# Kernel optimization log

Measured on AMD Instinct MI355X. Metric: run time of the kernel, lower is better.

The kernel has to match this reference:

```python
import jax, jax.numpy as jnp
import numpy as np

N = 100000   # nodes
E = 1000000  # edges (before self-loops)
IN = 128     # in_channel
HID = 32     # hidden_channels
H1 = 8       # in_head
OUT = 40     # out_channel
NEG_SLOPE = 0.2


def setup_inputs() -> dict:
    key = jax.random.key(0)
    ks = jax.random.split(key, 12)
    s = 0.05
    return {
        "x0": jax.random.normal(ks[0], (N, IN), jnp.float32),
        "W1": jax.random.normal(ks[1], (IN, H1 * HID), jnp.float32) * s,
        "att_src1": jax.random.normal(ks[2], (H1, HID), jnp.float32) * s,
        "att_dst1": jax.random.normal(ks[3], (H1, HID), jnp.float32) * s,
        "b1": jnp.zeros((H1 * HID,), jnp.float32),
        "W2": jax.random.normal(ks[4], (H1 * HID, 1 * HID), jnp.float32) * s,
        "att_src2": jax.random.normal(ks[5], (1, HID), jnp.float32) * s,
        "att_dst2": jax.random.normal(ks[6], (1, HID), jnp.float32) * s,
        "b2": jnp.zeros((HID,), jnp.float32),
        "linW": jax.random.normal(ks[7], (HID, OUT), jnp.float32) * s,
        "linb": jnp.zeros((OUT,), jnp.float32),
        "edge_index": jax.random.randint(ks[8], (2, E), 0, N, dtype=jnp.int64),
    }


def gat_conv(x, src, dst, W, att_src, att_dst, bias, concat):
    # PyG GATConv (eval mode): per-head linear, edge attention, dst-softmax, scatter-add
    H, C = att_src.shape
    h = (x @ W).reshape(N, H, C)                       # [N,H,C]
    a_src = jnp.sum(h * att_src[None], axis=-1)        # [N,H]
    a_dst = jnp.sum(h * att_dst[None], axis=-1)        # [N,H]
    alpha = jax.nn.leaky_relu(a_src[src] + a_dst[dst], NEG_SLOPE)  # [Etot,H]
    m = jax.ops.segment_max(alpha, dst, num_segments=N)           # [N,H]
    ea = jnp.exp(alpha - m[dst])
    denom = jax.ops.segment_sum(ea, dst, num_segments=N)
    w = ea / jnp.clip(denom, 1e-16, None)[dst]          # [Etot,H]
    out = jax.ops.segment_sum(w[:, :, None] * h[src], dst, num_segments=N)  # [N,H,C]
    out = out.reshape(N, H * C) if concat else jnp.mean(out, axis=1)
    return out + bias


def reference(x0, W1, att_src1, att_dst1, b1, W2, att_src2, att_dst2, b2, linW, linb, edge_index):
    # add self-loops (PyG add_self_loops=True default)
    loop = jnp.arange(N, dtype=edge_index.dtype)
    src = jnp.concatenate([edge_index[0], loop])
    dst = jnp.concatenate([edge_index[1], loop])
    # dropout layers are no-ops in eval mode
    x1 = gat_conv(x0, src, dst, W1, att_src1, att_dst1, b1, concat=True)   # [N, 8*HID]
    x2 = jax.nn.relu(x1)
    x2 = gat_conv(x2, src, dst, W2, att_src2, att_dst2, b2, concat=False)  # [N, HID]
    return x2 @ linW + linb                                                 # [N, OUT]
```

## Files before the change

### kernel.cpp

```cpp
#include <hip/hip_runtime.h>

#define N 100000
#define E 1000000
#define ETOT 1100000
#define NB1 391
#define NBE 4297

typedef __attribute__((ext_vector_type(8))) short bf16x8;
typedef __attribute__((ext_vector_type(4))) float f32x4;

__device__ __forceinline__ float lrelu(float x) { return x > 0.f ? x : 0.2f * x; }
__device__ __forceinline__ unsigned short f2b(float x) {
    unsigned u = __float_as_uint(x);
    return (unsigned short)((u + 0x7FFFu + ((u >> 16) & 1u)) >> 16);
}
__device__ __forceinline__ float b2f(unsigned short v) {
    return __uint_as_float(((unsigned)v) << 16);
}

__global__ __launch_bounds__(256) void prep_kernel(const int* __restrict__ ei,
                                                   int* __restrict__ hist,
                                                   const float* __restrict__ W1,
                                                   const float* __restrict__ W2,
                                                   const float* __restrict__ att_src1,
                                                   const float* __restrict__ att_dst1,
                                                   unsigned short* __restrict__ W1T,
                                                   unsigned short* __restrict__ W2T) {
    const int b = blockIdx.x;
    const int t = threadIdx.x;
    if (b < NBE) {
        const int e = b * 256 + t;
        if (e < ETOT) {
            int d = (e < E) ? ei[E + e] : (e - E);
            atomicAdd(&hist[d], 1);
        }
        return;
    }
    const int bb = b - NBE;
    if (bb < 128) {
        W1T[(size_t)t * 128 + bb] = f2b(W1[(size_t)bb * 256 + t]);
    } else if (bb < 160) {
        int n = bb - 128;
        W2T[(size_t)n * 256 + t] = f2b(W2[(size_t)t * 32 + n]);
    } else {
        int idx = (bb - 160) * 256 + t;
        int col = idx >> 7;
        int k = idx & 127;
        int h = col & 7;
        const float* att = (col < 8) ? att_src1 : att_dst1;
        float acc = 0.f;
#pragma unroll 8
        for (int j = 0; j < 32; j++) acc += W1[(size_t)k * 256 + h * 32 + j] * att[h * 32 + j];
        W1T[(size_t)(256 + col) * 128 + k] = f2b(acc);
    }
}

__global__ __launch_bounds__(256) void scan1_kernel(const int* __restrict__ hist,
                                                    int* __restrict__ rofs,
                                                    int* __restrict__ bsum) {
    __shared__ int sm[256];
    const int t = threadIdx.x;
    const int i = blockIdx.x * 256 + t;
    int v = (i < N) ? hist[i] : 0;
    sm[t] = v;
    __syncthreads();
#pragma unroll
    for (int off = 1; off < 256; off <<= 1) {
        int x = (t >= off) ? sm[t - off] : 0;
        __syncthreads();
        sm[t] += x;
        __syncthreads();
    }
    if (i < N) rofs[i] = sm[t] - v;
    if (t == 255) bsum[blockIdx.x] = sm[255];
}

__global__ __launch_bounds__(512) void scan2_kernel(int* __restrict__ bsum) {
    __shared__ int sm[512];
    const int t = threadIdx.x;
    int v = (t < NB1) ? bsum[t] : 0;
    sm[t] = v;
    __syncthreads();
#pragma unroll
    for (int off = 1; off < 512; off <<= 1) {
        int x = (t >= off) ? sm[t - off] : 0;
        __syncthreads();
        sm[t] += x;
        __syncthreads();
    }
    if (t < NB1) bsum[t] = sm[t] - v;
}

__global__ __launch_bounds__(256) void scan3_kernel(int* __restrict__ rofs,
                                                    const int* __restrict__ bsum,
                                                    int* __restrict__ cursor) {
    const int i = blockIdx.x * 256 + threadIdx.x;
    if (i < N) {
        int r = rofs[i] + bsum[blockIdx.x];
        rofs[i] = r;
        cursor[i] = r;
    }
    if (i == 0) rofs[N] = ETOT;
}

__global__ __launch_bounds__(256) void scatter_kernel(const int* __restrict__ ei,
                                                      int* __restrict__ cursor,
                                                      int* __restrict__ esrc) {
    const int e = blockIdx.x * 256 + threadIdx.x;
    if (e >= ETOT) return;
    int s, d;
    if (e < E) { s = ei[e]; d = ei[E + e]; } else { s = d = e - E; }
    int pos = atomicAdd(&cursor[d], 1);
    esrc[pos] = s;
}

__global__ __launch_bounds__(256) void gemm1_kernel(const float* __restrict__ x0,
                                                    const unsigned short* __restrict__ W1T,
                                                    unsigned short* __restrict__ h1,
                                                    float* __restrict__ a_src,
                                                    float* __restrict__ a_dst) {
    const int wv = threadIdx.x >> 6;
    const int lane = threadIdx.x & 63;
    const int quad = lane >> 4, c = lane & 15;
    const int base_m = blockIdx.x * 128 + wv * 32;
    bf16x8 af[2][4];
#pragma unroll
    for (int mt = 0; mt < 2; mt++) {
        int row = base_m + mt * 16 + c;
        int rowc = row < N ? row : N - 1;
        const float* ap = x0 + (size_t)rowc * 128 + quad * 8;
#pragma unroll
        for (int ks = 0; ks < 4; ks++) {
            float4 lo = *(const float4*)(ap + ks * 32);
            float4 hi = *(const float4*)(ap + ks * 32 + 4);
            bf16x8 f;
            f[0] = (short)f2b(lo.x); f[1] = (short)f2b(lo.y);
            f[2] = (short)f2b(lo.z); f[3] = (short)f2b(lo.w);
            f[4] = (short)f2b(hi.x); f[5] = (short)f2b(hi.y);
            f[6] = (short)f2b(hi.z); f[7] = (short)f2b(hi.w);
            af[mt][ks] = f;
        }
    }
    for (int nt = 0; nt < 17; nt++) {
        f32x4 acc0 = {0.f, 0.f, 0.f, 0.f};
        f32x4 acc1 = {0.f, 0.f, 0.f, 0.f};
#pragma unroll
        for (int ks = 0; ks < 4; ks++) {
            bf16x8 bf = *(const bf16x8*)(W1T + (size_t)(nt * 16 + c) * 128 + ks * 32 + quad * 8);
            acc0 = __builtin_amdgcn_mfma_f32_16x16x32_bf16(af[0][ks], bf, acc0, 0, 0, 0);
            acc1 = __builtin_amdgcn_mfma_f32_16x16x32_bf16(af[1][ks], bf, acc1, 0, 0, 0);
        }
        if (nt < 16) {
            const int col = nt * 16 + c;
#pragma unroll
            for (int r = 0; r < 4; r++) {
                int row0 = base_m + quad * 4 + r;
                if (row0 < N) h1[(size_t)row0 * 256 + col] = f2b(acc0[r]);
                int row1 = base_m + 16 + quad * 4 + r;
                if (row1 < N) h1[(size_t)row1 * 256 + col] = f2b(acc1[r]);
            }
        } else {
            float* dst = (c < 8) ? a_src : a_dst;
            int hh = c & 7;
#pragma unroll
            for (int r = 0; r < 4; r++) {
                int row0 = base_m + quad * 4 + r;
                if (row0 < N) dst[(size_t)row0 * 8 + hh] = acc0[r];
                int row1 = base_m + 16 + quad * 4 + r;
                if (row1 < N) dst[(size_t)row1 * 8 + hh] = acc1[r];
            }
        }
    }
}

__global__ __launch_bounds__(256) void seg1_kernel(const int* __restrict__ esrc,
                                                   const int* __restrict__ rofs,
                                                   const float* __restrict__ a_src,
                                                   const float* __restrict__ a_dst,
                                                   const unsigned short* __restrict__ h1,
                                                   const float* __restrict__ b1,
                                                   unsigned short* __restrict__ x2) {
    const int n = (blockIdx.x * 256 + threadIdx.x) >> 6;
    const int lane = threadIdx.x & 63;
    const int h = lane >> 3;
    const int rs = rofs[n], re = rofs[n + 1];
    const float ad = a_dst[(size_t)n * 8 + h];
    float d0 = 0.f, d1 = 0.f, d2 = 0.f, d3 = 0.f;
    float4 A0 = {0, 0, 0, 0}, A1 = {0, 0, 0, 0}, A2 = {0, 0, 0, 0}, A3 = {0, 0, 0, 0};
    for (int j0 = rs; j0 < re; j0 += 4) {
        const int cl = re - 1;
        int s0 = esrc[j0];
        int s1 = esrc[j0 + 1 < re ? j0 + 1 : cl];
        int s2 = esrc[j0 + 2 < re ? j0 + 2 : cl];
        int s3 = esrc[j0 + 3 < re ? j0 + 3 : cl];
        float as0 = a_src[(size_t)s0 * 8 + h];
        float as1 = a_src[(size_t)s1 * 8 + h];
        float as2 = a_src[(size_t)s2 * 8 + h];
        float as3 = a_src[(size_t)s3 * 8 + h];
        ushort4 hb0 = ((const ushort4*)(h1 + (size_t)s0 * 256))[lane];
        ushort4 hb1 = ((const ushort4*)(h1 + (size_t)s1 * 256))[lane];
        ushort4 hb2 = ((const ushort4*)(h1 + (size_t)s2 * 256))[lane];
        ushort4 hb3 = ((const ushort4*)(h1 + (size_t)s3 * 256))[lane];
        float w0 = __expf(lrelu(as0 + ad));
        float w1 = (j0 + 1 < re) ? __expf(lrelu(as1 + ad)) : 0.f;
        float w2 = (j0 + 2 < re) ? __expf(lrelu(as2 + ad)) : 0.f;
        float w3 = (j0 + 3 < re) ? __expf(lrelu(as3 + ad)) : 0.f;
        d0 += w0; d1 += w1; d2 += w2; d3 += w3;
        A0.x += w0 * b2f(hb0.x); A0.y += w0 * b2f(hb0.y); A0.z += w0 * b2f(hb0.z); A0.w += w0 * b2f(hb0.w);
        A1.x += w1 * b2f(hb1.x); A1.y += w1 * b2f(hb1.y); A1.z += w1 * b2f(hb1.z); A1.w += w1 * b2f(hb1.w);
        A2.x += w2 * b2f(hb2.x); A2.y += w2 * b2f(hb2.y); A2.z += w2 * b2f(hb2.z); A2.w += w2 * b2f(hb2.w);
        A3.x += w3 * b2f(hb3.x); A3.y += w3 * b2f(hb3.y); A3.z += w3 * b2f(hb3.z); A3.w += w3 * b2f(hb3.w);
    }
    float den = (d0 + d1) + (d2 + d3);
    float4 acc;
    acc.x = (A0.x + A1.x) + (A2.x + A3.x);
    acc.y = (A0.y + A1.y) + (A2.y + A3.y);
    acc.z = (A0.z + A1.z) + (A2.z + A3.z);
    acc.w = (A0.w + A1.w) + (A2.w + A3.w);
    const float inv = 1.0f / den;
    float4 bb = ((const float4*)b1)[lane];
    float vx = acc.x * inv + bb.x, vy = acc.y * inv + bb.y;
    float vz = acc.z * inv + bb.z, vw = acc.w * inv + bb.w;
    vx = vx > 0.f ? vx : 0.f; vy = vy > 0.f ? vy : 0.f;
    vz = vz > 0.f ? vz : 0.f; vw = vw > 0.f ? vw : 0.f;
    ushort4 o = {f2b(vx), f2b(vy), f2b(vz), f2b(vw)};
    ((ushort4*)(x2 + (size_t)n * 256))[lane] = o;
}

__global__ __launch_bounds__(256) void gemm2_kernel(const unsigned short* __restrict__ x2,
                                                    const unsigned short* __restrict__ W2T,
                                                    const float* __restrict__ att_src2,
                                                    const float* __restrict__ att_dst2,
                                                    unsigned short* __restrict__ h2,
                                                    float* __restrict__ a_src2,
                                                    float* __restrict__ a_dst2) {
    const int wv = threadIdx.x >> 6;
    const int lane = threadIdx.x & 63;
    const int quad = lane >> 4, c = lane & 15;
    const int base_m = blockIdx.x * 128 + wv * 32;
    f32x4 acc[2][2] = {{{0, 0, 0, 0}, {0, 0, 0, 0}}, {{0, 0, 0, 0}, {0, 0, 0, 0}}};
#pragma unroll
    for (int ks = 0; ks < 8; ks++) {
        bf16x8 b0 = *(const bf16x8*)(W2T + (size_t)c * 256 + ks * 32 + quad * 8);
        bf16x8 b1 = *(const bf16x8*)(W2T + (size_t)(16 + c) * 256 + ks * 32 + quad * 8);
#pragma unroll
        for (int mt = 0; mt < 2; mt++) {
            int row = base_m + mt * 16 + c;
            int rowc = row < N ? row : N - 1;
            bf16x8 a = *(const bf16x8*)(x2 + (size_t)rowc * 256 + ks * 32 + quad * 8);
            acc[mt][0] = __builtin_amdgcn_mfma_f32_16x16x32_bf16(a, b0, acc[mt][0], 0, 0, 0);
            acc[mt][1] = __builtin_amdgcn_mfma_f32_16x16x32_bf16(a, b1, acc[mt][1], 0, 0, 0);
        }
    }
    float as0 = att_src2[c], as1 = att_src2[16 + c];
    float ad0 = att_dst2[c], ad1 = att_dst2[16 + c];
#pragma unroll
    for (int mt = 0; mt < 2; mt++) {
#pragma unroll
        for (int r = 0; r < 4; r++) {
            int row = base_m + mt * 16 + quad * 4 + r;
            float v0 = acc[mt][0][r], v1 = acc[mt][1][r];
            float ps = v0 * as0 + v1 * as1;
            float pd = v0 * ad0 + v1 * ad1;
#pragma unroll
            for (int off = 1; off < 16; off <<= 1) {
                ps += __shfl_xor(ps, off, 64);
                pd += __shfl_xor(pd, off, 64);
            }
            if (row < N) {
                h2[(size_t)row * 32 + c] = f2b(v0);
                h2[(size_t)row * 32 + 16 + c] = f2b(v1);
                if (c == 0) { a_src2[row] = ps; a_dst2[row] = pd; }
            }
        }
    }
}

__global__ __launch_bounds__(256) void seg2_kernel(const int* __restrict__ esrc,
                                                   const int* __restrict__ rofs,
                                                   const float* __restrict__ a_src2,
                                                   const float* __restrict__ a_dst2,
                                                   const unsigned short* __restrict__ h2,
                                                   const float* __restrict__ b2,
                                                   const float* __restrict__ linW,
                                                   const float* __restrict__ linb,
                                                   float* __restrict__ out) {
    __shared__ float lws[32 * 40];
    __shared__ float vbuf[8][32];
    const int t = threadIdx.x;
    for (int i = t; i < 1280; i += 256) lws[i] = linW[i];
    const int n8 = t >> 5;
    const int c = t & 31;
    const int n = blockIdx.x * 8 + n8;
    const int rs = rofs[n], re = rofs[n + 1];
    const float ad = a_dst2[n];
    float d[8] = {0, 0, 0, 0, 0, 0, 0, 0};
    float A[8] = {0, 0, 0, 0, 0, 0, 0, 0};
    for (int j0 = rs; j0 < re; j0 += 8) {
        int sidx[8];
#pragma unroll
        for (int k = 0; k < 8; k++) {
            int j = j0 + k;
            sidx[k] = esrc[j < re ? j : re - 1];
        }
        unsigned short hb[8];
        float as[8];
#pragma unroll
        for (int k = 0; k < 8; k++) {
            hb[k] = h2[(size_t)sidx[k] * 32 + c];
            as[k] = a_src2[sidx[k]];
        }
#pragma unroll
        for (int k = 0; k < 8; k++) {
            float w = (j0 + k < re) ? __expf(lrelu(as[k] + ad)) : 0.f;
            d[k] += w;
            A[k] += w * b2f(hb[k]);
        }
    }
    float den = ((d[0] + d[1]) + (d[2] + d[3])) + ((d[4] + d[5]) + (d[6] + d[7]));
    float acc = ((A[0] + A[1]) + (A[2] + A[3])) + ((A[4] + A[5]) + (A[6] + A[7]));
    vbuf[n8][c] = acc / den + b2[c];
    __syncthreads();
    for (int idx = t; idx < 320; idx += 256) {
        int nn = idx / 40, o = idx - nn * 40;
        float s = linb[o];
#pragma unroll
        for (int ci = 0; ci < 32; ci++) s += vbuf[nn][ci] * lws[ci * 40 + o];
        out[(size_t)blockIdx.x * 320 + idx] = s;
    }
}

extern "C" void kernel_launch(void* const* d_in, const int* in_sizes, int n_in,
                              void* d_out, int out_size, void* d_ws, size_t ws_size,
                              hipStream_t stream) {
    const float* x0       = (const float*)d_in[0];
    const float* W1       = (const float*)d_in[1];
    const float* att_src1 = (const float*)d_in[2];
    const float* att_dst1 = (const float*)d_in[3];
    const float* b1       = (const float*)d_in[4];
    const float* W2       = (const float*)d_in[5];
    const float* att_src2 = (const float*)d_in[6];
    const float* att_dst2 = (const float*)d_in[7];
    const float* b2       = (const float*)d_in[8];
    const float* linW     = (const float*)d_in[9];
    const float* linb     = (const float*)d_in[10];
    const int*   ei       = (const int*)d_in[11];
    float* out = (float*)d_out;
    float* ws  = (float*)d_ws;

    unsigned short* h1   = (unsigned short*)ws;
    unsigned short* x2   = (unsigned short*)(ws + 12800000);
    float* a_src1        = ws + 25600000;
    float* a_dst1        = ws + 26400000;
    unsigned short* h2   = (unsigned short*)(ws + 27200000);
    float* a_src2        = ws + 28800000;
    float* a_dst2        = ws + 28900000;
    unsigned short* W1T  = (unsigned short*)(ws + 29000000);
    unsigned short* W2T  = (unsigned short*)(ws + 29020000);
    int*   hist          = (int*)(ws + 29030000);
    int*   rofs          = (int*)(ws + 29130000);
    int*   cursor        = (int*)(ws + 29240000);
    int*   bsum          = (int*)(ws + 29340000);
    int*   esrc          = (int*)(ws + 29341000);

    hipMemsetAsync(hist, 0, (size_t)N * 4, stream);

    prep_kernel<<<NBE + 168, 256, 0, stream>>>(ei, hist, W1, W2, att_src1, att_dst1, W1T, W2T);
    scan1_kernel<<<NB1, 256, 0, stream>>>(hist, rofs, bsum);
    scan2_kernel<<<1, 512, 0, stream>>>(bsum);
    scan3_kernel<<<NB1, 256, 0, stream>>>(rofs, bsum, cursor);
    scatter_kernel<<<(ETOT + 255) / 256, 256, 0, stream>>>(ei, cursor, esrc);

    gemm1_kernel<<<(N + 127) / 128, 256, 0, stream>>>(x0, W1T, h1, a_src1, a_dst1);
    seg1_kernel<<<N / 4, 256, 0, stream>>>(esrc, rofs, a_src1, a_dst1, h1, b1, x2);
    gemm2_kernel<<<(N + 127) / 128, 256, 0, stream>>>(x2, W2T, att_src2, att_dst2, h2, a_src2, a_dst2);
    seg2_kernel<<<N / 8, 256, 0, stream>>>(esrc, rofs, a_src2, a_dst2, h2, b2, linW, linb, out);
}
```

Measured before the change: 437.4 us.

## Cooperatively load edge indices and attention weights across lanes in segment kernels

```diff
diff --git a/kernel.cpp b/kernel.cpp
--- a/kernel.cpp
+++ b/kernel.cpp
@@ -182,41 +182,42 @@
                                                    unsigned short* __restrict__ x2) {
     const int n = (blockIdx.x * 256 + threadIdx.x) >> 6;
     const int lane = threadIdx.x & 63;
-    const int h = lane >> 3;
-    const int rs = rofs[n], re = rofs[n + 1];
-    const float ad = a_dst[(size_t)n * 8 + h];
-    float d0 = 0.f, d1 = 0.f, d2 = 0.f, d3 = 0.f;
-    float4 A0 = {0, 0, 0, 0}, A1 = {0, 0, 0, 0}, A2 = {0, 0, 0, 0}, A3 = {0, 0, 0, 0};
-    for (int j0 = rs; j0 < re; j0 += 4) {
-        const int cl = re - 1;
-        int s0 = esrc[j0];
-        int s1 = esrc[j0 + 1 < re ? j0 + 1 : cl];
-        int s2 = esrc[j0 + 2 < re ? j0 + 2 : cl];
-        int s3 = esrc[j0 + 3 < re ? j0 + 3 : cl];
-        float as0 = a_src[(size_t)s0 * 8 + h];
-        float as1 = a_src[(size_t)s1 * 8 + h];
-        float as2 = a_src[(size_t)s2 * 8 + h];
-        float as3 = a_src[(size_t)s3 * 8 + h];
-        ushort4 hb0 = ((const ushort4*)(h1 + (size_t)s0 * 256))[lane];
-        ushort4 hb1 = ((const ushort4*)(h1 + (size_t)s1 * 256))[lane];
-        ushort4 hb2 = ((const ushort4*)(h1 + (size_t)s2 * 256))[lane];
-        ushort4 hb3 = ((const ushort4*)(h1 + (size_t)s3 * 256))[lane];
-        float w0 = __expf(lrelu(as0 + ad));
-        float w1 = (j0 + 1 < re) ? __expf(lrelu(as1 + ad)) : 0.f;
-        float w2 = (j0 + 2 < re) ? __expf(lrelu(as2 + ad)) : 0.f;
-        float w3 = (j0 + 3 < re) ? __expf(lrelu(as3 + ad)) : 0.f;
-        d0 += w0; d1 += w1; d2 += w2; d3 += w3;
-        A0.x += w0 * b2f(hb0.x); A0.y += w0 * b2f(hb0.y); A0.z += w0 * b2f(hb0.z); A0.w += w0 * b2f(hb0.w);
-        A1.x += w1 * b2f(hb1.x); A1.y += w1 * b2f(hb1.y); A1.z += w1 * b2f(hb1.z); A1.w += w1 * b2f(hb1.w);
-        A2.x += w2 * b2f(hb2.x); A2.y += w2 * b2f(hb2.y); A2.z += w2 * b2f(hb2.z); A2.w += w2 * b2f(hb2.w);
-        A3.x += w3 * b2f(hb3.x); A3.y += w3 * b2f(hb3.y); A3.z += w3 * b2f(hb3.z); A3.w += w3 * b2f(hb3.w);
-    }
-    float den = (d0 + d1) + (d2 + d3);
-    float4 acc;
-    acc.x = (A0.x + A1.x) + (A2.x + A3.x);
-    acc.y = (A0.y + A1.y) + (A2.y + A3.y);
-    acc.z = (A0.z + A1.z) + (A2.z + A3.z);
-    acc.w = (A0.w + A1.w) + (A2.w + A3.w);
+    const int e_pa = lane >> 3;
+    const int h_pa = lane & 7;
+    const int hB = lane >> 3;
+    const int rs = __builtin_amdgcn_readfirstlane(rofs[n]);
+    const int re = __builtin_amdgcn_readfirstlane(rofs[n + 1]);
+    const float ad_pa = a_dst[(size_t)n * 8 + h_pa];
+    float dsum = 0.f;
+    float4 Aa = {0, 0, 0, 0}, Ab = {0, 0, 0, 0};
+    for (int j0 = rs; j0 < re; j0 += 8) {
+        int jm = j0 + e_pa;
+        int jc = jm < re ? jm : re - 1;
+        int s8 = esrc[jc];
+        float av = a_src[(size_t)s8 * 8 + h_pa];
+        float ex = __expf(lrelu(av + ad_pa));
+        float w = (jm < re) ? ex : 0.f;
+        dsum += w;
+#pragma unroll
+        for (int e = 0; e < 8; e++) {
+            if ((e & 3) == 0 && j0 + e >= re) break;
+            float wb = __shfl(w, e * 8 + hB, 64);
+            int se = __builtin_amdgcn_readlane(s8, e * 8);
+            ushort4 hb = ((const ushort4*)(h1 + (size_t)se * 256))[lane];
+            if (e & 1) {
+                Ab.x += wb * b2f(hb.x); Ab.y += wb * b2f(hb.y);
+                Ab.z += wb * b2f(hb.z); Ab.w += wb * b2f(hb.w);
+            } else {
+                Aa.x += wb * b2f(hb.x); Aa.y += wb * b2f(hb.y);
+                Aa.z += wb * b2f(hb.z); Aa.w += wb * b2f(hb.w);
+            }
+        }
+    }
+    dsum += __shfl_xor(dsum, 8, 64);
+    dsum += __shfl_xor(dsum, 16, 64);
+    dsum += __shfl_xor(dsum, 32, 64);
+    float den = __shfl(dsum, hB, 64);
+    float4 acc = {Aa.x + Ab.x, Aa.y + Ab.y, Aa.z + Ab.z, Aa.w + Ab.w};
     const float inv = 1.0f / den;
     float4 bb = ((const float4*)b1)[lane];
     float vx = acc.x * inv + bb.x, vy = acc.y * inv + bb.y;
@@ -286,47 +287,50 @@
                                                    const float* __restrict__ linb,
                                                    float* __restrict__ out) {
     __shared__ float lws[32 * 40];
-    __shared__ float vbuf[8][32];
+    __shared__ float vbuf[4][32];
     const int t = threadIdx.x;
     for (int i = t; i < 1280; i += 256) lws[i] = linW[i];
-    const int n8 = t >> 5;
-    const int c = t & 31;
-    const int n = blockIdx.x * 8 + n8;
-    const int rs = rofs[n], re = rofs[n + 1];
+    const int wv = t >> 6;
+    const int lane = t & 63;
+    const int n = blockIdx.x * 4 + wv;
+    const int rs = __builtin_amdgcn_readfirstlane(rofs[n]);
+    const int re = __builtin_amdgcn_readfirstlane(rofs[n + 1]);
     const float ad = a_dst2[n];
-    float d[8] = {0, 0, 0, 0, 0, 0, 0, 0};
-    float A[8] = {0, 0, 0, 0, 0, 0, 0, 0};
-    for (int j0 = rs; j0 < re; j0 += 8) {
-        int sidx[8];
-#pragma unroll
-        for (int k = 0; k < 8; k++) {
-            int j = j0 + k;
-            sidx[k] = esrc[j < re ? j : re - 1];
-        }
-        unsigned short hb[8];
-        float as[8];
-#pragma unroll
-        for (int k = 0; k < 8; k++) {
-            hb[k] = h2[(size_t)sidx[k] * 32 + c];
-            as[k] = a_src2[sidx[k]];
-        }
-#pragma unroll
-        for (int k = 0; k < 8; k++) {
-            float w = (j0 + k < re) ? __expf(lrelu(as[k] + ad)) : 0.f;
-            d[k] += w;
-            A[k] += w * b2f(hb[k]);
-        }
-    }
-    float den = ((d[0] + d[1]) + (d[2] + d[3])) + ((d[4] + d[5]) + (d[6] + d[7]));
-    float acc = ((A[0] + A[1]) + (A[2] + A[3])) + ((A[4] + A[5]) + (A[6] + A[7]));
-    vbuf[n8][c] = acc / den + b2[c];
+    const int ec = lane >> 5;
+    const int c = lane & 31;
+    float dsum = 0.f;
+    float A = 0.f;
+    for (int j0 = rs; j0 < re; j0 += 64) {
+        int jm = j0 + lane;
+        int jc = jm < re ? jm : re - 1;
+        int s = esrc[jc];
+        float av = a_src2[s];
+        float ex = __expf(lrelu(av + ad));
+        float w = (jm < re) ? ex : 0.f;
+        dsum += w;
+        int cnt = re - j0; if (cnt > 64) cnt = 64;
+        for (int e = 0; e < cnt; e += 2) {
+            float wb = __shfl(w, e + ec, 64);
+            int sb = __shfl(s, e + ec, 64);
+            unsigned short hb = h2[(size_t)sb * 32 + c];
+            A += wb * b2f(hb);
+        }
+    }
+    A += __shfl_xor(A, 32, 64);
+    dsum += __shfl_xor(dsum, 1, 64);
+    dsum += __shfl_xor(dsum, 2, 64);
+    dsum += __shfl_xor(dsum, 4, 64);
+    dsum += __shfl_xor(dsum, 8, 64);
+    dsum += __shfl_xor(dsum, 16, 64);
+    dsum += __shfl_xor(dsum, 32, 64);
+    if (lane < 32) vbuf[wv][c] = A / dsum + b2[c];
     __syncthreads();
-    for (int idx = t; idx < 320; idx += 256) {
+    for (int idx = t; idx < 160; idx += 256) {
         int nn = idx / 40, o = idx - nn * 40;
-        float s = linb[o];
-#pragma unroll
-        for (int ci = 0; ci < 32; ci++) s += vbuf[nn][ci] * lws[ci * 40 + o];
-        out[(size_t)blockIdx.x * 320 + idx] = s;
+        float s2 = linb[o];
+#pragma unroll
+        for (int ci = 0; ci < 32; ci++) s2 += vbuf[nn][ci] * lws[ci * 40 + o];
+        out[(size_t)blockIdx.x * 160 + idx] = s2;
     }
 }
 
@@ -374,5 +378,5 @@
     gemm1_kernel<<<(N + 127) / 128, 256, 0, stream>>>(x0, W1T, h1, a_src1, a_dst1);
     seg1_kernel<<<N / 4, 256, 0, stream>>>(esrc, rofs, a_src1, a_dst1, h1, b1, x2);
     gemm2_kernel<<<(N + 127) / 128, 256, 0, stream>>>(x2, W2T, att_src2, att_dst2, h2, a_src2, a_dst2);
-    seg2_kernel<<<N / 8, 256, 0, stream>>>(esrc, rofs, a_src2, a_dst2, h2, b2, linW, linb, out);
-}
+    seg2_kernel<<<N / 4, 256, 0, stream>>>(esrc, rofs, a_src2, a_dst2, h2, b2, linW, linb, out);
+}
```

Result: slower. 455.5 us (+4.1%).

## Merge edge scatter with layer-1 GEMM and cooperatively compute seg1 attention weights

Applied to the files above, without the earlier changes.

```diff
diff --git a/kernel.cpp b/kernel.cpp
--- a/kernel.cpp
+++ b/kernel.cpp
@@ -5,6 +5,7 @@
 #define ETOT 1100000
 #define NB1 391
 #define NBE 4297
+#define NBG 782
 
 typedef __attribute__((ext_vector_type(8))) short bf16x8;
 typedef __attribute__((ext_vector_type(4))) float f32x4;
@@ -103,26 +104,28 @@
     if (i == 0) rofs[N] = ETOT;
 }
 
-__global__ __launch_bounds__(256) void scatter_kernel(const int* __restrict__ ei,
-                                                      int* __restrict__ cursor,
-                                                      int* __restrict__ esrc) {
-    const int e = blockIdx.x * 256 + threadIdx.x;
-    if (e >= ETOT) return;
-    int s, d;
-    if (e < E) { s = ei[e]; d = ei[E + e]; } else { s = d = e - E; }
-    int pos = atomicAdd(&cursor[d], 1);
-    esrc[pos] = s;
-}
-
-__global__ __launch_bounds__(256) void gemm1_kernel(const float* __restrict__ x0,
-                                                    const unsigned short* __restrict__ W1T,
-                                                    unsigned short* __restrict__ h1,
-                                                    float* __restrict__ a_src,
-                                                    float* __restrict__ a_dst) {
+__global__ __launch_bounds__(256) void sg_kernel(const int* __restrict__ ei,
+                                                 int* __restrict__ cursor,
+                                                 int* __restrict__ esrc,
+                                                 const float* __restrict__ x0,
+                                                 const unsigned short* __restrict__ W1T,
+                                                 unsigned short* __restrict__ h1,
+                                                 float* __restrict__ a_src,
+                                                 float* __restrict__ a_dst) {
+    if (blockIdx.x < NBE) {
+        const int e = blockIdx.x * 256 + threadIdx.x;
+        if (e < ETOT) {
+            int s, d;
+            if (e < E) { s = ei[e]; d = ei[E + e]; } else { s = d = e - E; }
+            int pos = atomicAdd(&cursor[d], 1);
+            esrc[pos] = s;
+        }
+        return;
+    }
     const int wv = threadIdx.x >> 6;
     const int lane = threadIdx.x & 63;
     const int quad = lane >> 4, c = lane & 15;
-    const int base_m = blockIdx.x * 128 + wv * 32;
+    const int base_m = (blockIdx.x - NBE) * 128 + wv * 32;
     bf16x8 af[2][4];
 #pragma unroll
     for (int mt = 0; mt < 2; mt++) {
@@ -182,41 +185,41 @@
                                                    unsigned short* __restrict__ x2) {
     const int n = (blockIdx.x * 256 + threadIdx.x) >> 6;
     const int lane = threadIdx.x & 63;
-    const int h = lane >> 3;
-    const int rs = rofs[n], re = rofs[n + 1];
-    const float ad = a_dst[(size_t)n * 8 + h];
-    float d0 = 0.f, d1 = 0.f, d2 = 0.f, d3 = 0.f;
-    float4 A0 = {0, 0, 0, 0}, A1 = {0, 0, 0, 0}, A2 = {0, 0, 0, 0}, A3 = {0, 0, 0, 0};
-    for (int j0 = rs; j0 < re; j0 += 4) {
-        const int cl = re - 1;
-        int s0 = esrc[j0];
-        int s1 = esrc[j0 + 1 < re ? j0 + 1 : cl];
-        int s2 = esrc[j0 + 2 < re ? j0 + 2 : cl];
-        int s3 = esrc[j0 + 3 < re ? j0 + 3 : cl];
-        float as0 = a_src[(size_t)s0 * 8 + h];
-        float as1 = a_src[(size_t)s1 * 8 + h];
-        float as2 = a_src[(size_t)s2 * 8 + h];
-        float as3 = a_src[(size_t)s3 * 8 + h];
-        ushort4 hb0 = ((const ushort4*)(h1 + (size_t)s0 * 256))[lane];
-        ushort4 hb1 = ((const ushort4*)(h1 + (size_t)s1 * 256))[lane];
-        ushort4 hb2 = ((const ushort4*)(h1 + (size_t)s2 * 256))[lane];
-        ushort4 hb3 = ((const ushort4*)(h1 + (size_t)s3 * 256))[lane];
-        float w0 = __expf(lrelu(as0 + ad));
-        float w1 = (j0 + 1 < re) ? __expf(lrelu(as1 + ad)) : 0.f;
-        float w2 = (j0 + 2 < re) ? __expf(lrelu(as2 + ad)) : 0.f;
-        float w3 = (j0 + 3 < re) ? __expf(lrelu(as3 + ad)) : 0.f;
-        d0 += w0; d1 += w1; d2 += w2; d3 += w3;
-        A0.x += w0 * b2f(hb0.x); A0.y += w0 * b2f(hb0.y); A0.z += w0 * b2f(hb0.z); A0.w += w0 * b2f(hb0.w);
-        A1.x += w1 * b2f(hb1.x); A1.y += w1 * b2f(hb1.y); A1.z += w1 * b2f(hb1.z); A1.w += w1 * b2f(hb1.w);
-        A2.x += w2 * b2f(hb2.x); A2.y += w2 * b2f(hb2.y); A2.z += w2 * b2f(hb2.z); A2.w += w2 * b2f(hb2.w);
-        A3.x += w3 * b2f(hb3.x); A3.y += w3 * b2f(hb3.y); A3.z += w3 * b2f(hb3.z); A3.w += w3 * b2f(hb3.w);
-    }
-    float den = (d0 + d1) + (d2 + d3);
-    float4 acc;
-    acc.x = (A0.x + A1.x) + (A2.x + A3.x);
-    acc.y = (A0.y + A1.y) + (A2.y + A3.y);
-    acc.z = (A0.z + A1.z) + (A2.z + A3.z);
-    acc.w = (A0.w + A1.w) + (A2.w + A3.w);
+    const int e_pa = lane >> 3;
+    const int h_pa = lane & 7;
+    const int hB = lane >> 3;
+    const int rs = __builtin_amdgcn_readfirstlane(rofs[n]);
+    const int re = __builtin_amdgcn_readfirstlane(rofs[n + 1]);
+    const float ad_pa = a_dst[(size_t)n * 8 + h_pa];
+    float dsum = 0.f;
+    float4 Aa = {0, 0, 0, 0}, Ab = {0, 0, 0, 0};
+    for (int j0 = rs; j0 < re; j0 += 8) {
+        int jm = j0 + e_pa;
+        int jc = jm < re ? jm : re - 1;
+        int s8 = esrc[jc];
+        float av = a_src[(size_t)s8 * 8 + h_pa];
+        float ex = __expf(lrelu(av + ad_pa));
+        float w = (jm < re) ? ex : 0.f;
+        dsum += w;
+#pragma unroll
+        for (int e = 0; e < 8; e++) {
+            float wb = __shfl(w, e * 8 + hB, 64);
+            int se = __builtin_amdgcn_readlane(s8, e * 8);
+            ushort4 hb = ((const ushort4*)(h1 + (size_t)se * 256))[lane];
+            if (e & 1) {
+                Ab.x += wb * b2f(hb.x); Ab.y += wb * b2f(hb.y);
+                Ab.z += wb * b2f(hb.z); Ab.w += wb * b2f(hb.w);
+            } else {
+                Aa.x += wb * b2f(hb.x); Aa.y += wb * b2f(hb.y);
+                Aa.z += wb * b2f(hb.z); Aa.w += wb * b2f(hb.w);
+            }
+        }
+    }
+    dsum += __shfl_xor(dsum, 8, 64);
+    dsum += __shfl_xor(dsum, 16, 64);
+    dsum += __shfl_xor(dsum, 32, 64);
+    float den = __shfl(dsum, hB, 64);
+    float4 acc = {Aa.x + Ab.x, Aa.y + Ab.y, Aa.z + Ab.z, Aa.w + Ab.w};
     const float inv = 1.0f / den;
     float4 bb = ((const float4*)b1)[lane];
     float vx = acc.x * inv + bb.x, vy = acc.y * inv + bb.y;
@@ -369,9 +372,9 @@
     scan1_kernel<<<NB1, 256, 0, stream>>>(hist, rofs, bsum);
     scan2_kernel<<<1, 512, 0, stream>>>(bsum);
     scan3_kernel<<<NB1, 256, 0, stream>>>(rofs, bsum, cursor);
-    scatter_kernel<<<(ETOT + 255) / 256, 256, 0, stream>>>(ei, cursor, esrc);
-
-    gemm1_kernel<<<(N + 127) / 128, 256, 0, stream>>>(x0, W1T, h1, a_src1, a_dst1);
+
+    sg_kernel<<<NBE + NBG, 256, 0, stream>>>(ei, cursor, esrc, x0, W1T, h1, a_src1, a_dst1);
+
     seg1_kernel<<<N / 4, 256, 0, stream>>>(esrc, rofs, a_src1, a_dst1, h1, b1, x2);
     gemm2_kernel<<<(N + 127) / 128, 256, 0, stream>>>(x2, W2T, att_src2, att_dst2, h2, a_src2, a_dst2);
     seg2_kernel<<<N / 8, 256, 0, stream>>>(esrc, rofs, a_src2, a_dst2, h2, b2, linW, linb, out);
```

Result: slower. 457.9 us (+4.7%).
